# Kernel optimization log

Measured on AMD Instinct MI355X. Metric: run time of the kernel, lower is better.

## Reference

```python
import jax, jax.numpy as jnp
import numpy as np

EPS = 1e-5
SCALES = jnp.array([7.0, 7.0, 4.0], dtype=jnp.float32)  # (W, H, T) per source buffer
OUT_T, OUT_H, OUT_W = 3, 5, 5


def _roi_align3d(feat, start, end):
    """feat: [C,T,H,W]; start/end: [3] = (x, y, t). One sample per bin (bin center),
    trilinear interpolation, out-of-bounds -> 0 (standard ROIAlign convention)."""
    C, T, H, W = feat.shape
    dt = feat.dtype

    def centers(s, e, n):
        b = (e - s) / n
        return s + (jnp.arange(n, dtype=dt) + 0.5) * b

    xc = centers(start[0], end[0], OUT_W)  # [Wo]
    yc = centers(start[1], end[1], OUT_H)  # [Ho]
    tc = centers(start[2], end[2], OUT_T)  # [To]

    def prep(c, size):
        valid = ((c >= -1.0) & (c <= size)).astype(dt)
        c = jnp.clip(c, 0.0, size - 1)
        lo = jnp.floor(c).astype(jnp.int32)
        hi = jnp.minimum(lo + 1, size - 1)
        f = c - lo.astype(dt)
        return (lo, hi), ((1.0 - f) * valid, f * valid)

    ti, tw = prep(tc, T)
    yi, yw = prep(yc, H)
    xi, xw = prep(xc, W)

    out = jnp.zeros((C, OUT_T, OUT_H, OUT_W), dtype=dt)
    for a in range(2):
        for b in range(2):
            for c in range(2):
                g = feat[:, ti[a][:, None, None], yi[b][None, :, None], xi[c][None, None, :]]
                w = tw[a][:, None, None] * yw[b][None, :, None] * xw[c][None, None, :]
                out = out + g * w
    return out


def setup_inputs() -> dict:
    key = jax.random.key(0)
    k0, k1, k2 = jax.random.split(key, 3)
    B, C, T, H, W = 128, 1024, 4, 7, 7
    R = 256
    x = jax.random.normal(k0, (B, C, T, H, W), jnp.float32)
    w1 = jax.random.normal(k1, (R, C), jnp.float32) / np.sqrt(C).astype(np.float32)
    w2 = jax.random.normal(k2, (6, R), jnp.float32) / np.sqrt(R).astype(np.float32)
    return dict(
        x=x, w1=w1,
        g1=jnp.ones((R,), jnp.float32), b1=jnp.zeros((R,), jnp.float32),
        m1=jnp.zeros((R,), jnp.float32), v1=jnp.ones((R,), jnp.float32),
        w2=w2,
        g2=jnp.ones((6,), jnp.float32), b2=jnp.zeros((6,), jnp.float32),
        m2=jnp.zeros((6,), jnp.float32), v2=jnp.ones((6,), jnp.float32),
    )


def reference(x, w1, g1, b1, m1, v1, w2, g2, b2, m2, v2):
    # roi head: conv1x1x1 -> BN(eval) -> HSwish -> global avgpool -> conv1x1x1 -> BN(eval)
    h = jnp.einsum('bcthw,rc->brthw', x, w1)
    s1 = (g1 / jnp.sqrt(v1 + EPS))
    h = (h - m1[None, :, None, None, None]) * s1[None, :, None, None, None] + b1[None, :, None, None, None]
    h = h * jnp.clip(h + 3.0, 0.0, 6.0) * (1.0 / 6.0)  # HSwish
    h = h.mean(axis=(2, 3, 4))                          # AvgPool3d over full (T,H,W) -> [B,R]
    logits = h @ w2.T
    logits = (logits - m2) * (g2 / jnp.sqrt(v2 + EPS)) + b2  # [B,6]
    raw = jax.nn.sigmoid(logits)
    roi_start = 0.5 * raw[:, :3] * SCALES              # (x1,y1,t1)
    roi_end = (1.0 - 0.5 * raw[:, 3:]) * SCALES        # (x2,y2,t2)
    return jax.vmap(_roi_align3d)(x, roi_start, roi_end)  # [B,C,3,5,5]
```

## Files before the change

kernel.cpp:

```cpp
#include <hip/hip_runtime.h>

typedef __bf16 bf16x8 __attribute__((ext_vector_type(8)));
typedef float f32x4 __attribute__((ext_vector_type(4)));

#define EPS_F 1e-5f

__device__ __forceinline__ void gload_lds16(const void* g, void* l) {
    __builtin_amdgcn_global_load_lds(
        (const __attribute__((address_space(1))) unsigned int*)g,
        (__attribute__((address_space(3))) unsigned int*)l, 16, 0, 0);
}

__global__ __launch_bounds__(256) void k_pack_x(
    const float* __restrict__ x, __bf16* __restrict__ xt)
{
    __shared__ float xs[32][204];
    const int b = blockIdx.x, kt = blockIdx.y, tid = threadIdx.x;
    const float* src = x + ((size_t)b * 1024 + (size_t)kt * 32) * 196;
#pragma unroll
    for (int k = 0; k < 7; k++) {
        const int i4 = tid + k * 256;
        if (i4 < 1568) {
            const int c = i4 / 49, pq = i4 % 49;
            const float4 v = *(const float4*)(src + c * 196 + pq * 4);
            *(float4*)&xs[c][pq * 4] = v;
        }
    }
    __syncthreads();
    __bf16* dst = xt + (size_t)(b * 32 + kt) * 196 * 32;
#pragma unroll
    for (int k = 0; k < 4; k++) {
        const int it = tid + k * 256;
        if (it < 784) {
            const int p = it >> 2, g = it & 3;
            bf16x8 o;
#pragma unroll
            for (int j = 0; j < 8; j++) o[j] = (__bf16)xs[g * 8 + j][p];
            *(bf16x8*)(dst + (size_t)p * 32 + g * 8) = o;
        }
    }
}

__global__ __launch_bounds__(256) void k_pack_w1(
    const float* __restrict__ w1, __bf16* __restrict__ w1t)
{
    const int it = blockIdx.x * 256 + threadIdx.x;
    const int kt = it >> 10, rem = it & 1023, r = rem >> 2, g = rem & 3;
    const float* s = w1 + (size_t)r * 1024 + kt * 32 + g * 8;
    bf16x8 o;
#pragma unroll
    for (int j = 0; j < 8; j++) o[j] = (__bf16)s[j];
    *(bf16x8*)(w1t + (size_t)it * 8) = o;
}

__global__ __launch_bounds__(512) void k_gemm_pool(
    const __bf16* __restrict__ xt,
    const __bf16* __restrict__ w1t,
    const float* __restrict__ g1,
    const float* __restrict__ b1,
    const float* __restrict__ m1,
    const float* __restrict__ v1,
    float* __restrict__ pooled_part)
{
    __shared__ __bf16 Alds[2][4096];
    __shared__ __bf16 Blds[2][8192];
    __shared__ float pool_lds[2][256];

    const int b   = blockIdx.x;
    const int mc  = blockIdx.y;
    const int tid = threadIdx.x;
    const int wave = tid >> 6, lane = tid & 63;
    const int wm = wave >> 2, wn = wave & 3;
    const int q  = lane >> 4, ln = lane & 15;
    const int nm = (wm == 0) ? 4 : 3;

    f32x4 acc[4][4];
#pragma unroll
    for (int i = 0; i < 4; i++)
#pragma unroll
        for (int j = 0; j < 4; j++) acc[i][j] = (f32x4){0.f, 0.f, 0.f, 0.f};

    const __bf16* xa = xt + ((size_t)b * 32 * 196 + (size_t)mc * 112) * 32 + tid * 8;
    const __bf16* wb = w1t + tid * 8;

    auto issue = [&](int kt, int buf) {
        gload_lds16(xa + (size_t)kt * (196 * 32), &Alds[buf][wave * 512]);
        gload_lds16(wb + (size_t)kt * 8192,       &Blds[buf][wave * 512]);
        gload_lds16(wb + (size_t)kt * 8192 + 4096, &Blds[buf][4096 + wave * 512]);
    };

    issue(0, 0);

    for (int t = 0; t < 32; ++t) {
        const int cur = t & 1;
        if (t < 31) {
            issue(t + 1, cur ^ 1);
            asm volatile("s_waitcnt vmcnt(3)" ::: "memory");
        } else {
            asm volatile("s_waitcnt vmcnt(0)" ::: "memory");
        }
        __builtin_amdgcn_s_barrier();
        __builtin_amdgcn_sched_barrier(0);
        bf16x8 bfr[4];
#pragma unroll
        for (int ni = 0; ni < 4; ni++)
            bfr[ni] = *(const bf16x8*)&Blds[cur][(((wn * 4 + ni) * 16 + ln) * 32) + q * 8];
#pragma unroll
        for (int mi = 0; mi < 4; mi++) {
            if (mi < nm) {
                const bf16x8 af =
                    *(const bf16x8*)&Alds[cur][(((wm * 4 + mi) * 16 + ln) * 32) + q * 8];
#pragma unroll
                for (int ni = 0; ni < 4; ni++)
                    acc[mi][ni] = __builtin_amdgcn_mfma_f32_16x16x32_bf16(
                        af, bfr[ni], acc[mi][ni], 0, 0, 0);
            }
        }
        __builtin_amdgcn_sched_barrier(0);
        __builtin_amdgcn_s_barrier();
    }

    float psum[4] = {0.f, 0.f, 0.f, 0.f};
#pragma unroll
    for (int ni = 0; ni < 4; ni++) {
        const int r = (wn * 4 + ni) * 16 + ln;
        const float s1 = g1[r] * rsqrtf(v1[r] + EPS_F);
        const float mu = m1[r];
        const float be = b1[r];
#pragma unroll
        for (int mi = 0; mi < 4; mi++) {
            if (mi < nm) {
#pragma unroll
                for (int i = 0; i < 4; i++) {
                    const int m = mc * 112 + (wm * 4 + mi) * 16 + q * 4 + i;
                    if (m < 196) {
                        float v = acc[mi][ni][i];
                        v = (v - mu) * s1 + be;
                        const float g = fminf(fmaxf(v + 3.f, 0.f), 6.f);
                        psum[ni] += v * g * (1.f / 6.f);
                    }
                }
            }
        }
    }
#pragma unroll
    for (int ni = 0; ni < 4; ni++) {
        psum[ni] += __shfl_xor(psum[ni], 16, 64);
        psum[ni] += __shfl_xor(psum[ni], 32, 64);
    }
    if (lane < 16) {
#pragma unroll
        for (int ni = 0; ni < 4; ni++)
            pool_lds[wm][(wn * 4 + ni) * 16 + lane] = psum[ni];
    }
    __syncthreads();
    if (tid < 256)
        pooled_part[(size_t)mc * (128 * 256) + b * 256 + tid] =
            (pool_lds[0][tid] + pool_lds[1][tid]) * (1.f / 196.f);
}

__global__ __launch_bounds__(64) void k_logits(
    const float* __restrict__ pooled_part,
    const float* __restrict__ w2,
    const float* __restrict__ g2,
    const float* __restrict__ b2,
    const float* __restrict__ m2,
    const float* __restrict__ v2,
    float* __restrict__ roi)
{
    const int b = blockIdx.x, t = threadIdx.x;
    const float4 pa = ((const float4*)(pooled_part + b * 256))[t];
    const float4 pb = ((const float4*)(pooled_part + 128 * 256 + b * 256))[t];
    float4 p4;
    p4.x = pa.x + pb.x; p4.y = pa.y + pb.y;
    p4.z = pa.z + pb.z; p4.w = pa.w + pb.w;
    float part[6];
#pragma unroll
    for (int j = 0; j < 6; j++) {
        const float4 w = *(const float4*)(w2 + j * 256 + t * 4);
        part[j] = p4.x * w.x + p4.y * w.y + p4.z * w.z + p4.w * w.w;
    }
#pragma unroll
    for (int j = 0; j < 6; j++)
#pragma unroll
        for (int off = 32; off >= 1; off >>= 1)
            part[j] += __shfl_xor(part[j], off, 64);
    if (t == 0) {
        const float SC[3] = {7.f, 7.f, 4.f};
        float raw[6];
#pragma unroll
        for (int j = 0; j < 6; j++) {
            float l = part[j];
            const float s = g2[j] * rsqrtf(v2[j] + EPS_F);
            l = (l - m2[j]) * s + b2[j];
            raw[j] = 1.f / (1.f + expf(-l));
        }
#pragma unroll
        for (int d = 0; d < 3; d++) {
            roi[b * 6 + d]     = 0.5f * raw[d] * SC[d];
            roi[b * 6 + 3 + d] = (1.f - 0.5f * raw[3 + d]) * SC[d];
        }
    }
}

__device__ __forceinline__ void prep1(float s, float e, int n, int size, int i,
                                      int& lo, int& hi, float& w0, float& w1)
{
    const float bsz = (e - s) / (float)n;
    float c = s + ((float)i + 0.5f) * bsz;
    const float valid = (c >= -1.f && c <= (float)size) ? 1.f : 0.f;
    c = fminf(fmaxf(c, 0.f), (float)(size - 1));
    lo = (int)floorf(c);
    hi = min(lo + 1, size - 1);
    const float f = c - (float)lo;
    w0 = (1.f - f) * valid;
    w1 = f * valid;
}

__global__ __launch_bounds__(256) void k_roi(
    const float* __restrict__ x,
    const float* __restrict__ roi,
    float* __restrict__ out)
{
    __shared__ float xs[32 * 200];
    __shared__ int   soff[8][80];
    __shared__ float swt[8][80];

    const int b = blockIdx.x, c0 = blockIdx.y * 32;
    const int tid = threadIdx.x;

    const float* xb = x + ((size_t)b * 1024 + c0) * 196;
#pragma unroll
    for (int k = 0; k < 7; k++) {
        const int i4 = tid + k * 256;
        if (i4 < 1568) {
            const int c = i4 / 49, pq = i4 % 49;
            const float4 v = *(const float4*)(xb + c * 196 + pq * 4);
            *(float4*)&xs[c * 200 + pq * 4] = v;
        }
    }
    if (tid < 75) {
        const int po = tid;
        const int to = po / 25, rem = po % 25, yo = rem / 5, xo = rem % 5;
        const float sx = roi[b * 6 + 0], ex = roi[b * 6 + 3];
        const float sy = roi[b * 6 + 1], ey = roi[b * 6 + 4];
        const float st = roi[b * 6 + 2], et = roi[b * 6 + 5];
        int tl, th, yl, yh, xl, xh;
        float tw0, tw1, yw0, yw1, xw0, xw1;
        prep1(st, et, 3, 4, to, tl, th, tw0, tw1);
        prep1(sy, ey, 5, 7, yo, yl, yh, yw0, yw1);
        prep1(sx, ex, 5, 7, xo, xl, xh, xw0, xw1);
#pragma unroll
        for (int s = 0; s < 8; s++) {
            const int   ti = (s & 4) ? th : tl;
            const int   yi = (s & 2) ? yh : yl;
            const int   xi = (s & 1) ? xh : xl;
            const float w = ((s & 4) ? tw1 : tw0) *
                            ((s & 2) ? yw1 : yw0) *
                            ((s & 1) ? xw1 : xw0);
            soff[s][po] = ti * 49 + yi * 7 + xi;
            swt[s][po]  = w;
        }
    }
    __syncthreads();

    const size_t obase = ((size_t)b * 1024 + c0) * 75;
#pragma unroll
    for (int k = 0; k < 10; k++) {
        const int e = tid + k * 256;
        if (e < 2400) {
            const int c = e / 75, po = e % 75;
            const float* row = &xs[c * 200];
            float v = 0.f;
#pragma unroll
            for (int s = 0; s < 8; s++)
                v += swt[s][po] * row[soff[s][po]];
            out[obase + e] = v;
        }
    }
}

extern "C" void kernel_launch(void* const* d_in, const int* in_sizes, int n_in,
                              void* d_out, int out_size, void* d_ws, size_t ws_size,
                              hipStream_t stream)
{
    const float* x  = (const float*)d_in[0];
    const float* w1 = (const float*)d_in[1];
    const float* g1 = (const float*)d_in[2];
    const float* b1 = (const float*)d_in[3];
    const float* m1 = (const float*)d_in[4];
    const float* v1 = (const float*)d_in[5];
    const float* w2 = (const float*)d_in[6];
    const float* g2 = (const float*)d_in[7];
    const float* b2 = (const float*)d_in[8];
    const float* m2 = (const float*)d_in[9];
    const float* v2 = (const float*)d_in[10];

    char* wsb = (char*)d_ws;
    __bf16* xt     = (__bf16*)wsb;
    __bf16* w1t    = (__bf16*)(wsb + 51388416);
    float*  pooled = (float*)(wsb + 51912704);
    float*  roi    = (float*)(wsb + 52174848);
    float*  out    = (float*)d_out;

    k_pack_w1<<<128, 256, 0, stream>>>(w1, w1t);
    k_pack_x<<<dim3(128, 32), 256, 0, stream>>>(x, xt);
    k_gemm_pool<<<dim3(128, 2), 512, 0, stream>>>(xt, w1t, g1, b1, m1, v1, pooled);
    k_logits<<<128, 64, 0, stream>>>(pooled, w2, g2, b2, m2, v2, roi);
    k_roi<<<dim3(128, 32), 256, 0, stream>>>(x, roi, out);
}
```

Baseline: 248.8 us.

## Merge pack kernels, fold logits into ROI kernel, deepen GEMM prefetch to four stages

The w1 and x packing kernels become a single launch, with an extra grid column handling w1. The logits/sigmoid stage now runs inside each ROI block, which recomputes the ROI box from the pooled features, so one launch and the roi round trip go away. The GEMM moves from double to quad buffered LDS with three tiles in flight and one barrier per iteration. The cost is redundant logits work in every ROI block (32x per batch), more LDS per GEMM block, and reliance on the single barrier to avoid overwriting a buffer that is still being read.

```diff
diff --git a/kernel.cpp b/kernel.cpp
--- a/kernel.cpp
+++ b/kernel.cpp
@@ -11,11 +11,25 @@
         (__attribute__((address_space(3))) unsigned int*)l, 16, 0, 0);
 }
 
-__global__ __launch_bounds__(256) void k_pack_x(
-    const float* __restrict__ x, __bf16* __restrict__ xt)
-{
+__global__ __launch_bounds__(256) void k_pack(
+    const float* __restrict__ x, const float* __restrict__ w1,
+    __bf16* __restrict__ xt, __bf16* __restrict__ w1t)
+{
+    const int b = blockIdx.x, kt = blockIdx.y, tid = threadIdx.x;
+    if (b == 128) {
+#pragma unroll
+        for (int j = 0; j < 4; j++) {
+            const int it = kt * 1024 + tid + j * 256;
+            const int kk = it >> 10, rem = it & 1023, r = rem >> 2, g = rem & 3;
+            const float* s = w1 + (size_t)r * 1024 + kk * 32 + g * 8;
+            bf16x8 o;
+#pragma unroll
+            for (int e = 0; e < 8; e++) o[e] = (__bf16)s[e];
+            *(bf16x8*)(w1t + (size_t)it * 8) = o;
+        }
+        return;
+    }
     __shared__ float xs[32][204];
-    const int b = blockIdx.x, kt = blockIdx.y, tid = threadIdx.x;
     const float* src = x + ((size_t)b * 1024 + (size_t)kt * 32) * 196;
 #pragma unroll
     for (int k = 0; k < 7; k++) {
@@ -39,18 +53,6 @@
             *(bf16x8*)(dst + (size_t)p * 32 + g * 8) = o;
         }
     }
-}
-
-__global__ __launch_bounds__(256) void k_pack_w1(
-    const float* __restrict__ w1, __bf16* __restrict__ w1t)
-{
-    const int it = blockIdx.x * 256 + threadIdx.x;
-    const int kt = it >> 10, rem = it & 1023, r = rem >> 2, g = rem & 3;
-    const float* s = w1 + (size_t)r * 1024 + kt * 32 + g * 8;
-    bf16x8 o;
-#pragma unroll
-    for (int j = 0; j < 8; j++) o[j] = (__bf16)s[j];
-    *(bf16x8*)(w1t + (size_t)it * 8) = o;
 }
 
 __global__ __launch_bounds__(512) void k_gemm_pool(
@@ -62,8 +64,8 @@
     const float* __restrict__ v1,
     float* __restrict__ pooled_part)
 {
-    __shared__ __bf16 Alds[2][4096];
-    __shared__ __bf16 Blds[2][8192];
+    __shared__ __bf16 Alds[4][4096];
+    __shared__ __bf16 Blds[4][8192];
     __shared__ float pool_lds[2][256];
 
     const int b   = blockIdx.x;
@@ -85,22 +87,21 @@
 
     auto issue = [&](int kt, int buf) {
         gload_lds16(xa + (size_t)kt * (196 * 32), &Alds[buf][wave * 512]);
-        gload_lds16(wb + (size_t)kt * 8192,       &Blds[buf][wave * 512]);
+        gload_lds16(wb + (size_t)kt * 8192,        &Blds[buf][wave * 512]);
         gload_lds16(wb + (size_t)kt * 8192 + 4096, &Blds[buf][4096 + wave * 512]);
     };
 
-    issue(0, 0);
+    issue(0, 0); issue(1, 1); issue(2, 2);
 
     for (int t = 0; t < 32; ++t) {
-        const int cur = t & 1;
-        if (t < 31) {
-            issue(t + 1, cur ^ 1);
-            asm volatile("s_waitcnt vmcnt(3)" ::: "memory");
-        } else {
-            asm volatile("s_waitcnt vmcnt(0)" ::: "memory");
-        }
+        if (t < 30)       asm volatile("s_waitcnt vmcnt(6)" ::: "memory");
+        else if (t == 30) asm volatile("s_waitcnt vmcnt(3)" ::: "memory");
+        else              asm volatile("s_waitcnt vmcnt(0)" ::: "memory");
         __builtin_amdgcn_s_barrier();
         __builtin_amdgcn_sched_barrier(0);
+        if (t + 3 < 32) issue(t + 3, (t + 3) & 3);
+        __builtin_amdgcn_sched_barrier(0);
+        const int cur = t & 3;
         bf16x8 bfr[4];
 #pragma unroll
         for (int ni = 0; ni < 4; ni++)
@@ -116,8 +117,6 @@
                         af, bfr[ni], acc[mi][ni], 0, 0, 0);
             }
         }
-        __builtin_amdgcn_sched_barrier(0);
-        __builtin_amdgcn_s_barrier();
     }
 
     float psum[4] = {0.f, 0.f, 0.f, 0.f};
@@ -159,50 +158,6 @@
             (pool_lds[0][tid] + pool_lds[1][tid]) * (1.f / 196.f);
 }
 
-__global__ __launch_bounds__(64) void k_logits(
-    const float* __restrict__ pooled_part,
-    const float* __restrict__ w2,
-    const float* __restrict__ g2,
-    const float* __restrict__ b2,
-    const float* __restrict__ m2,
-    const float* __restrict__ v2,
-    float* __restrict__ roi)
-{
-    const int b = blockIdx.x, t = threadIdx.x;
-    const float4 pa = ((const float4*)(pooled_part + b * 256))[t];
-    const float4 pb = ((const float4*)(pooled_part + 128 * 256 + b * 256))[t];
-    float4 p4;
-    p4.x = pa.x + pb.x; p4.y = pa.y + pb.y;
-    p4.z = pa.z + pb.z; p4.w = pa.w + pb.w;
-    float part[6];
-#pragma unroll
-    for (int j = 0; j < 6; j++) {
-        const float4 w = *(const float4*)(w2 + j * 256 + t * 4);
-        part[j] = p4.x * w.x + p4.y * w.y + p4.z * w.z + p4.w * w.w;
-    }
-#pragma unroll
-    for (int j = 0; j < 6; j++)
-#pragma unroll
-        for (int off = 32; off >= 1; off >>= 1)
-            part[j] += __shfl_xor(part[j], off, 64);
-    if (t == 0) {
-        const float SC[3] = {7.f, 7.f, 4.f};
-        float raw[6];
-#pragma unroll
-        for (int j = 0; j < 6; j++) {
-            float l = part[j];
-            const float s = g2[j] * rsqrtf(v2[j] + EPS_F);
-            l = (l - m2[j]) * s + b2[j];
-            raw[j] = 1.f / (1.f + expf(-l));
-        }
-#pragma unroll
-        for (int d = 0; d < 3; d++) {
-            roi[b * 6 + d]     = 0.5f * raw[d] * SC[d];
-            roi[b * 6 + 3 + d] = (1.f - 0.5f * raw[3 + d]) * SC[d];
-        }
-    }
-}
-
 __device__ __forceinline__ void prep1(float s, float e, int n, int size, int i,
                                       int& lo, int& hi, float& w0, float& w1)
 {
@@ -219,12 +174,18 @@
 
 __global__ __launch_bounds__(256) void k_roi(
     const float* __restrict__ x,
-    const float* __restrict__ roi,
+    const float* __restrict__ pooled_part,
+    const float* __restrict__ w2,
+    const float* __restrict__ g2,
+    const float* __restrict__ b2,
+    const float* __restrict__ m2,
+    const float* __restrict__ v2,
     float* __restrict__ out)
 {
     __shared__ float xs[32 * 200];
     __shared__ int   soff[8][80];
     __shared__ float swt[8][80];
+    __shared__ float roi_s[6];
 
     const int b = blockIdx.x, c0 = blockIdx.y * 32;
     const int tid = threadIdx.x;
@@ -239,17 +200,45 @@
             *(float4*)&xs[c * 200 + pq * 4] = v;
         }
     }
+    if (tid < 64) {
+        const float4 pa = ((const float4*)(pooled_part + b * 256))[tid];
+        const float4 pb = ((const float4*)(pooled_part + 128 * 256 + b * 256))[tid];
+        float4 p4;
+        p4.x = pa.x + pb.x; p4.y = pa.y + pb.y;
+        p4.z = pa.z + pb.z; p4.w = pa.w + pb.w;
+        float part[6];
+#pragma unroll
+        for (int j = 0; j < 6; j++) {
+            const float4 w = *(const float4*)(w2 + j * 256 + tid * 4);
+            part[j] = p4.x * w.x + p4.y * w.y + p4.z * w.z + p4.w * w.w;
+        }
+#pragma unroll
+        for (int j = 0; j < 6; j++)
+#pragma unroll
+            for (int off = 32; off >= 1; off >>= 1)
+                part[j] += __shfl_xor(part[j], off, 64);
+        if (tid == 0) {
+            const float SC[3] = {7.f, 7.f, 4.f};
+#pragma unroll
+            for (int j = 0; j < 6; j++) {
+                float l = part[j];
+                const float s = g2[j] * rsqrtf(v2[j] + EPS_F);
+                l = (l - m2[j]) * s + b2[j];
+                const float raw = 1.f / (1.f + expf(-l));
+                roi_s[j] = (j < 3) ? 0.5f * raw * SC[j]
+                                   : (1.f - 0.5f * raw) * SC[j - 3];
+            }
+        }
+    }
+    __syncthreads();
     if (tid < 75) {
         const int po = tid;
         const int to = po / 25, rem = po % 25, yo = rem / 5, xo = rem % 5;
-        const float sx = roi[b * 6 + 0], ex = roi[b * 6 + 3];
-        const float sy = roi[b * 6 + 1], ey = roi[b * 6 + 4];
-        const float st = roi[b * 6 + 2], et = roi[b * 6 + 5];
         int tl, th, yl, yh, xl, xh;
         float tw0, tw1, yw0, yw1, xw0, xw1;
-        prep1(st, et, 3, 4, to, tl, th, tw0, tw1);
-        prep1(sy, ey, 5, 7, yo, yl, yh, yw0, yw1);
-        prep1(sx, ex, 5, 7, xo, xl, xh, xw0, xw1);
+        prep1(roi_s[2], roi_s[5], 3, 4, to, tl, th, tw0, tw1);
+        prep1(roi_s[1], roi_s[4], 5, 7, yo, yl, yh, yw0, yw1);
+        prep1(roi_s[0], roi_s[3], 5, 7, xo, xl, xh, xw0, xw1);
 #pragma unroll
         for (int s = 0; s < 8; s++) {
             const int   ti = (s & 4) ? th : tl;
@@ -300,12 +289,9 @@
     __bf16* xt     = (__bf16*)wsb;
     __bf16* w1t    = (__bf16*)(wsb + 51388416);
     float*  pooled = (float*)(wsb + 51912704);
-    float*  roi    = (float*)(wsb + 52174848);
     float*  out    = (float*)d_out;
 
-    k_pack_w1<<<128, 256, 0, stream>>>(w1, w1t);
-    k_pack_x<<<dim3(128, 32), 256, 0, stream>>>(x, xt);
+    k_pack<<<dim3(129, 32), 256, 0, stream>>>(x, w1, xt, w1t);
     k_gemm_pool<<<dim3(128, 2), 512, 0, stream>>>(xt, w1t, g1, b1, m1, v1, pooled);
-    k_logits<<<128, 64, 0, stream>>>(pooled, w2, g2, b2, m2, v2, roi);
-    k_roi<<<dim3(128, 32), 256, 0, stream>>>(x, roi, out);
-}
+    k_roi<<<dim3(128, 32), 256, 0, stream>>>(x, pooled, w2, g2, b2, m2, v2, out);
+}
```

New measurement: 249.9 us. No clear change (+0.4%).
